# Optimization experiments

Hardware: AMD Instinct MI355X
Metric: run time of the kernel (lower is better)

## Reference

```python
import jax, jax.numpy as jnp
import numpy as np

EXPERT_NUM = 64
EXPERT_USE = 8
AUX_LOSS_LAMBDA = 0.01


def setup_inputs() -> dict:
    key = jax.random.key(0)
    k1, k2 = jax.random.split(key)
    h = jax.random.normal(k1, (4, 4096, 2048), dtype=jnp.float32)
    # nn.Linear(embed_dim, expert_num) weight: [expert_num, embed_dim], ~U(-1/sqrt(d), 1/sqrt(d))
    bound = 1.0 / np.sqrt(2048.0)
    W = jax.random.uniform(k2, (EXPERT_NUM, 2048), dtype=jnp.float32,
                           minval=-bound, maxval=bound)
    return {"h": h, "W": W}


def reference(h, W):
    b, s, d = h.shape
    hf = h.reshape(-1, d)                              # [b*s, d]
    logits = jnp.einsum('nd,ed->ne', hf, W)            # [b*s, E]
    scores = jax.nn.softmax(logits, axis=-1)           # [b*s, E]
    expert_scores, expert_ids = jax.lax.top_k(scores, EXPERT_USE)  # [b*s, k]
    expert_weight = expert_scores / jnp.sum(expert_scores, axis=-1, keepdims=True)
    # L2 load-balance aux loss (training mode, lambda > 0)
    seq_probs = scores.reshape(b, s, EXPERT_NUM).mean(axis=1)      # [b, E]
    aux_loss = jnp.mean(jnp.sum(seq_probs ** 2, axis=-1)) * EXPERT_NUM * AUX_LOSS_LAMBDA
    return expert_ids, expert_weight, aux_loss
```

## Files before the change

### kernel.cpp

```cpp
#include <hip/hip_runtime.h>
#include <math.h>

#define NTOK 16384
#define DIM 2048
#define NEXP 64
#define TOPK 8
#define BT 64
#define KC 64
#define NCHUNK (DIM / KC)
#define PADK 68
#define NBLK (NTOK / BT)
#define EPW 4

typedef float f2 __attribute__((ext_vector_type(2)));
typedef float f4 __attribute__((ext_vector_type(4)));

__device__ __forceinline__ f2 pk_mul_sv(f2 bs, f2 av) {
    f2 d; asm("v_pk_mul_f32 %0, %1, %2" : "=v"(d) : "s"(bs), "v"(av)); return d;
}
__device__ __forceinline__ f2 pk_add(f2 a, f2 b) {
    f2 d; asm("v_pk_add_f32 %0, %1, %2" : "=v"(d) : "v"(a), "v"(b)); return d;
}

__global__ __launch_bounds__(1024, 1) void moe_gate_np(
    const float* __restrict__ h, const float* __restrict__ W,
    float* __restrict__ out, float* __restrict__ wsum)
{
#pragma clang fp contract(off)
    __shared__ float sA[2][BT * PADK];
    __shared__ float lg[BT][NEXP + 2];

    const int tid  = threadIdx.x;
    const int lane = tid & 63;
    const int wv   = tid >> 6;
    const int blk  = blockIdx.x;
    const long tok0 = (long)blk * BT;
    const float* hA = h + tok0 * DIM;

    const int e0 = __builtin_amdgcn_readfirstlane(wv) * EPW;
    const float* wb = W + (long)e0 * DIM;

    const int rs = tid >> 4;
    const int cs = (tid & 15) * 4;

    f4 pa = *(const f4*)(hA + (long)rs * DIM + cs);
    *(f4*)&sA[0][rs * PADK + cs] = pa;
    pa = *(const f4*)(hA + (long)rs * DIM + KC + cs);

    f2 a01[EPW], a23[EPW];
    #pragma unroll
    for (int j = 0; j < EPW; ++j) { a01[j] = (f2)(0.f); a23[j] = (f2)(0.f); }

    for (int kc = 0; kc < NCHUNK; ++kc) {
        __syncthreads();
        const int cur = kc & 1;
        if (kc + 1 < NCHUNK)
            *(f4*)&sA[cur ^ 1][rs * PADK + cs] = pa;
        if (kc + 2 < NCHUNK)
            pa = *(const f4*)(hA + (long)rs * DIM + (long)(kc + 2) * KC + cs);

        #pragma unroll
        for (int s = 0; s < 4; ++s) {
            const int kb = kc * KC + s * 16;

            f4 B[EPW][4];
            #pragma unroll
            for (int j = 0; j < EPW; ++j)
                #pragma unroll
                for (int q = 0; q < 4; ++q)
                    B[j][q] = *(const f4*)(wb + (long)j * DIM + kb + 4 * q);

            f4 af[4];
            const float* ab = &sA[cur][lane * PADK + s * 16];
            #pragma unroll
            for (int v = 0; v < 4; ++v) af[v] = *(const f4*)(ab + 4 * v);

            f2 alo[4], ahi[4];
            #pragma unroll
            for (int v = 0; v < 4; ++v) {
                alo[v] = __builtin_shufflevector(af[v], af[v], 0, 1);
                ahi[v] = __builtin_shufflevector(af[v], af[v], 2, 3);
            }

            #pragma unroll
            for (int j = 0; j < EPW; ++j) {
                f2 blo[4], bhi[4];
                #pragma unroll
                for (int v = 0; v < 4; ++v) {
                    blo[v] = __builtin_shufflevector(B[j][v], B[j][v], 0, 1);
                    bhi[v] = __builtin_shufflevector(B[j][v], B[j][v], 2, 3);
                }
                f2 x;
                x = pk_add(pk_mul_sv(blo[3], alo[3]), a01[j]);
                x = pk_add(pk_mul_sv(blo[2], alo[2]), x);
                x = pk_add(pk_mul_sv(blo[1], alo[1]), x);
                a01[j] = pk_add(pk_mul_sv(blo[0], alo[0]), x);
                x = pk_add(pk_mul_sv(bhi[3], ahi[3]), a23[j]);
                x = pk_add(pk_mul_sv(bhi[2], ahi[2]), x);
                x = pk_add(pk_mul_sv(bhi[1], ahi[1]), x);
                a23[j] = pk_add(pk_mul_sv(bhi[0], ahi[0]), x);
            }
        }
    }

    #pragma unroll
    for (int j = 0; j < EPW; ++j) {
        f2 s2 = pk_add(a01[j], a23[j]);
        lg[lane][e0 + j] = s2.x + s2.y;
    }
    __syncthreads();

    float auxacc = 0.f;

    for (int tt = 0; tt < 4; ++tt) {
        const int t = wv * 4 + tt;
        const float s = lg[t][lane];

        float m = s;
        #pragma unroll
        for (int off = 32; off >= 1; off >>= 1)
            m = fmaxf(m, __shfl_xor(m, off));

        const float p = expf(s - m);
        lg[t][lane] = p;
        __asm__ volatile("" ::: "memory");

        float r0s = lg[t][0], r1s = lg[t][1], r2s = lg[t][2], r3s = lg[t][3];
        float r4s = lg[t][4], r5s = lg[t][5], r6s = lg[t][6], r7s = lg[t][7];
        #pragma unroll
        for (int i = 1; i < 8; ++i) {
            r0s += lg[t][8 * i + 0]; r1s += lg[t][8 * i + 1];
            r2s += lg[t][8 * i + 2]; r3s += lg[t][8 * i + 3];
            r4s += lg[t][8 * i + 4]; r5s += lg[t][8 * i + 5];
            r6s += lg[t][8 * i + 6]; r7s += lg[t][8 * i + 7];
        }
        const float S = ((r0s + r1s) + (r2s + r3s)) + ((r4s + r5s) + (r6s + r7s));

        const float score = p / S;
        auxacc += score;

        float cv = score;
        float myv = 0.f;
        int   myi = 0;
        #pragma unroll
        for (int i = 0; i < TOPK; ++i) {
            float v = cv;
            int idx = lane;
            #pragma unroll
            for (int off = 32; off >= 1; off >>= 1) {
                float v2 = __shfl_xor(v, off);
                int   i2 = __shfl_xor(idx, off);
                if (v2 > v || (v2 == v && i2 < idx)) { v = v2; idx = i2; }
            }
            if (lane == i)   { myv = v; myi = idx; }
            if (lane == idx) cv = -1.f;
        }

        float S8 = 0.f;
        #pragma unroll
        for (int r = 0; r < TOPK; ++r) S8 += __shfl(myv, r);

        if (lane < TOPK) {
            const long o = (tok0 + t) * TOPK + lane;
            out[o]                     = (float)myi;
            out[(long)NTOK * TOPK + o] = myv / S8;
        }
    }

    const int b = blk >> 6;
    atomicAdd(&wsum[b * NEXP + lane], auxacc);
}

__global__ void aux_finish(const float* __restrict__ wsum, float* __restrict__ out)
{
    const int lane = threadIdx.x;
    float a = 0.f;
    #pragma unroll
    for (int b = 0; b < 4; ++b) {
        const float v = wsum[b * NEXP + lane] * (1.0f / 4096.0f);
        a = fmaf(v, v, a);
    }
    #pragma unroll
    for (int off = 32; off >= 1; off >>= 1)
        a += __shfl_xor(a, off);
    if (lane == 0)
        out[2L * NTOK * TOPK] = a * 0.25f * (float)NEXP * 0.01f;
}

extern "C" void kernel_launch(void* const* d_in, const int* in_sizes, int n_in,
                              void* d_out, int out_size, void* d_ws, size_t ws_size,
                              hipStream_t stream) {
    const float* h = (const float*)d_in[0];
    const float* W = (const float*)d_in[1];
    float* out  = (float*)d_out;
    float* wsum = (float*)d_ws;

    hipMemsetAsync(d_ws, 0, 1024, stream);
    moe_gate_np<<<NBLK, 1024, 0, stream>>>(h, W, out, wsum);
    aux_finish<<<1, 64, 0, stream>>>(wsum, out);
}
```

Baseline: 143.0 us.

## Stage W tiles through LDS alongside h instead of scalar global loads

W is no longer read per wave through scalar global loads. It is now cooperatively loaded into a double-buffered LDS tile, with half the threads loading h rows and half loading W rows each chunk. The K chunk is halved to 32 so both tiles fit, and the packed multiply now takes B from VGPRs read out of LDS (broadcast reads). This trades scalar-cache W traffic for extra LDS reads and VGPR pressure, plus twice as many barriers per block.

```diff
diff --git a/kernel.cpp b/kernel.cpp
--- a/kernel.cpp
+++ b/kernel.cpp
@@ -6,17 +6,17 @@
 #define NEXP 64
 #define TOPK 8
 #define BT 64
-#define KC 64
+#define KC 32
 #define NCHUNK (DIM / KC)
-#define PADK 68
+#define PADK 36
 #define NBLK (NTOK / BT)
 #define EPW 4
 
 typedef float f2 __attribute__((ext_vector_type(2)));
 typedef float f4 __attribute__((ext_vector_type(4)));
 
-__device__ __forceinline__ f2 pk_mul_sv(f2 bs, f2 av) {
-    f2 d; asm("v_pk_mul_f32 %0, %1, %2" : "=v"(d) : "s"(bs), "v"(av)); return d;
+__device__ __forceinline__ f2 pk_mul(f2 a, f2 b) {
+    f2 d; asm("v_pk_mul_f32 %0, %1, %2" : "=v"(d) : "v"(a), "v"(b)); return d;
 }
 __device__ __forceinline__ f2 pk_add(f2 a, f2 b) {
     f2 d; asm("v_pk_add_f32 %0, %1, %2" : "=v"(d) : "v"(a), "v"(b)); return d;
@@ -28,6 +28,7 @@
 {
 #pragma clang fp contract(off)
     __shared__ float sA[2][BT * PADK];
+    __shared__ float sB[2][NEXP * PADK];
     __shared__ float lg[BT][NEXP + 2];
 
     const int tid  = threadIdx.x;
@@ -36,16 +37,20 @@
     const int blk  = blockIdx.x;
     const long tok0 = (long)blk * BT;
     const float* hA = h + tok0 * DIM;
-
-    const int e0 = __builtin_amdgcn_readfirstlane(wv) * EPW;
-    const float* wb = W + (long)e0 * DIM;
-
-    const int rs = tid >> 4;
-    const int cs = (tid & 15) * 4;
-
-    f4 pa = *(const f4*)(hA + (long)rs * DIM + cs);
-    *(f4*)&sA[0][rs * PADK + cs] = pa;
-    pa = *(const f4*)(hA + (long)rs * DIM + KC + cs);
+    const int e0 = wv * EPW;
+
+    const int sidx = tid & 511;
+    const int srow = sidx >> 3;
+    const int scol = (sidx & 7) * 4;
+    const bool isA = tid < 512;
+    const float* gsrc = isA ? (hA + (long)srow * DIM + scol)
+                            : (W  + (long)srow * DIM + scol);
+    float* l0 = isA ? &sA[0][srow * PADK + scol] : &sB[0][srow * PADK + scol];
+    float* l1 = isA ? &sA[1][srow * PADK + scol] : &sB[1][srow * PADK + scol];
+
+    f4 pa = *(const f4*)gsrc;
+    *(f4*)l0 = pa;
+    pa = *(const f4*)(gsrc + KC);
 
     f2 a01[EPW], a23[EPW];
     #pragma unroll
@@ -54,22 +59,14 @@
     for (int kc = 0; kc < NCHUNK; ++kc) {
         __syncthreads();
         const int cur = kc & 1;
+
         if (kc + 1 < NCHUNK)
-            *(f4*)&sA[cur ^ 1][rs * PADK + cs] = pa;
+            *(f4*)(cur ? l0 : l1) = pa;
         if (kc + 2 < NCHUNK)
-            pa = *(const f4*)(hA + (long)rs * DIM + (long)(kc + 2) * KC + cs);
-
-        #pragma unroll
-        for (int s = 0; s < 4; ++s) {
-            const int kb = kc * KC + s * 16;
-
-            f4 B[EPW][4];
-            #pragma unroll
-            for (int j = 0; j < EPW; ++j)
-                #pragma unroll
-                for (int q = 0; q < 4; ++q)
-                    B[j][q] = *(const f4*)(wb + (long)j * DIM + kb + 4 * q);
-
+            pa = *(const f4*)(gsrc + (long)(kc + 2) * KC);
+
+        #pragma unroll
+        for (int s = 0; s < 2; ++s) {
             f4 af[4];
             const float* ab = &sA[cur][lane * PADK + s * 16];
             #pragma unroll
@@ -82,23 +79,29 @@
                 ahi[v] = __builtin_shufflevector(af[v], af[v], 2, 3);
             }
 
+            const float* bb = &sB[cur][e0 * PADK + s * 16];
             #pragma unroll
             for (int j = 0; j < EPW; ++j) {
+                f4 Bf[4];
+                #pragma unroll
+                for (int v = 0; v < 4; ++v)
+                    Bf[v] = *(const f4*)(bb + j * PADK + 4 * v);
+
                 f2 blo[4], bhi[4];
                 #pragma unroll
                 for (int v = 0; v < 4; ++v) {
-                    blo[v] = __builtin_shufflevector(B[j][v], B[j][v], 0, 1);
-                    bhi[v] = __builtin_shufflevector(B[j][v], B[j][v], 2, 3);
+                    blo[v] = __builtin_shufflevector(Bf[v], Bf[v], 0, 1);
+                    bhi[v] = __builtin_shufflevector(Bf[v], Bf[v], 2, 3);
                 }
                 f2 x;
-                x = pk_add(pk_mul_sv(blo[3], alo[3]), a01[j]);
-                x = pk_add(pk_mul_sv(blo[2], alo[2]), x);
-                x = pk_add(pk_mul_sv(blo[1], alo[1]), x);
-                a01[j] = pk_add(pk_mul_sv(blo[0], alo[0]), x);
-                x = pk_add(pk_mul_sv(bhi[3], ahi[3]), a23[j]);
-                x = pk_add(pk_mul_sv(bhi[2], ahi[2]), x);
-                x = pk_add(pk_mul_sv(bhi[1], ahi[1]), x);
-                a23[j] = pk_add(pk_mul_sv(bhi[0], ahi[0]), x);
+                x = pk_add(pk_mul(blo[3], alo[3]), a01[j]);
+                x = pk_add(pk_mul(blo[2], alo[2]), x);
+                x = pk_add(pk_mul(blo[1], alo[1]), x);
+                a01[j] = pk_add(pk_mul(blo[0], alo[0]), x);
+                x = pk_add(pk_mul(bhi[3], ahi[3]), a23[j]);
+                x = pk_add(pk_mul(bhi[2], ahi[2]), x);
+                x = pk_add(pk_mul(bhi[1], ahi[1]), x);
+                a23[j] = pk_add(pk_mul(bhi[0], ahi[0]), x);
             }
         }
     }
```

Measured after the change: 153.8 us. +7.5%, slower.
